# Performance work log

Measured on AMD Instinct MI355X. Metric: run time of the kernel, lower is better.

## Reference

```python
import jax, jax.numpy as jnp
import numpy as np

NA, NB, NG = 40000, 200000, 500000
D, H, IN = 64, 64, 256  # feature dim, gMLP hidden, concat input dim (64+2*64+64)


def silu(x):
    return x * jax.nn.sigmoid(x)


def setup_inputs() -> dict:
    key = jax.random.key(0)
    ks = jax.random.split(key, 16)
    n = lambda k, sh, s=0.05: jax.random.normal(k, sh, jnp.float32) * s
    return {
        "atom_feas": n(ks[0], (NA, D), 1.0),
        "bond_feas": n(ks[1], (NB, D), 1.0),
        "bond_weights": jax.random.uniform(ks[2], (NB, D), jnp.float32),
        "angle_feas": n(ks[3], (NG, D), 1.0),
        "bond_graph": jax.random.randint(ks[4], (NG, 3), 0, NA, jnp.int64
                                          if jax.config.jax_enable_x64 else jnp.int32),
        "Wc1": n(ks[5], (IN, H)), "bc1": jnp.zeros((H,), jnp.float32),
        "Wc2": n(ks[6], (H, D)), "bc2": jnp.zeros((D,), jnp.float32),
        "Wg1": n(ks[7], (IN, H)), "bg1": jnp.zeros((H,), jnp.float32),
        "Wg2": n(ks[8], (H, D)), "bg2": jnp.zeros((D,), jnp.float32),
        "Wo": n(ks[9], (D, D)), "bo": jnp.zeros((D,), jnp.float32),
    }


def reference(atom_feas, bond_feas, bond_weights, angle_feas, bond_graph,
              Wc1, bc1, Wc2, bc2, Wg1, bg1, Wg2, bg2, Wo, bo):
    ci = bond_graph[:, 0]  # center atom index
    bi = bond_graph[:, 1]  # bond i index (also scatter target)
    bj = bond_graph[:, 2]  # bond j index
    # gather -> concat: [NG, 2*D + D + D] = [NG, 256]
    total = jnp.concatenate(
        [bond_feas[bi], bond_feas[bj], angle_feas, atom_feas[ci]], axis=1)
    # gated MLP (norm=None path): core = act(mlp_core(x)), gate = sigmoid(mlp_gate(x))
    core = silu(silu(total @ Wc1 + bc1) @ Wc2 + bc2)
    gate = jax.nn.sigmoid(silu(total @ Wg1 + bg1) @ Wg2 + bg2)
    upd = core * gate * bond_weights[bi] * bond_weights[bj]
    # scatter-sum back onto bonds (aggregate with average=False)
    agg = jax.ops.segment_sum(upd, bi, num_segments=bond_feas.shape[0])
    # mlp_out (single Linear) + residual; bond_norm is None
    return agg @ Wo + bo + bond_feas
```

## Files before the change

### kernel.cpp

```cpp
#include <hip/hip_runtime.h>
#include <hip/hip_bf16.h>

static constexpr int KD  = 64;
static constexpr int KH  = 64;

typedef __attribute__((ext_vector_type(8))) short bf16x8;
typedef __attribute__((ext_vector_type(4))) float f32x4;
typedef __attribute__((ext_vector_type(2))) float f32x2;

__device__ inline unsigned short f2bf(float f) {
  union { float f; unsigned u; } uf; uf.f = f;
  unsigned u = uf.u;
  return (unsigned short)((u + 0x7FFFu + ((u >> 16) & 1u)) >> 16);
}
__device__ inline float bf2f(unsigned short h) {
  union { unsigned u; float f; } x; x.u = ((unsigned)h) << 16; return x.f;
}
__device__ inline unsigned cvtpk_bf16(float lo, float hi) {
  unsigned r;
  asm("v_cvt_pk_bf16_f32 %0, %1, %2" : "=v"(r) : "v"(lo), "v"(hi));
  return r;
}
__device__ inline bf16x8 pack8(const float* p) {
  float4 lo = *(const float4*)p;
  float4 hi = *(const float4*)(p + 4);
  union { unsigned u[4]; bf16x8 v; } t;
  t.u[0] = cvtpk_bf16(lo.x, lo.y);
  t.u[1] = cvtpk_bf16(lo.z, lo.w);
  t.u[2] = cvtpk_bf16(hi.x, hi.y);
  t.u[3] = cvtpk_bf16(hi.z, hi.w);
  return t.v;
}
__device__ inline float sigm(float x) {
  return __builtin_amdgcn_rcpf(1.0f + __expf(-x));
}
__device__ inline float silu_(float x) { return x * sigm(x); }
__device__ inline unsigned pk_fp8x4(float a0, float a1, float a2, float a3) {
  int v = __builtin_amdgcn_cvt_pk_fp8_f32(a0, a1, 0, false);
  v = __builtin_amdgcn_cvt_pk_fp8_f32(a2, a3, v, true);
  return (unsigned)v;
}
template<bool HI>
__device__ inline f32x2 sum3_fp8(unsigned a, unsigned b, unsigned c) {
  f32x2 A = __builtin_amdgcn_cvt_pk_f32_fp8((int)a, HI);
  f32x2 B = __builtin_amdgcn_cvt_pk_f32_fp8((int)b, HI);
  f32x2 C = __builtin_amdgcn_cvt_pk_f32_fp8((int)c, HI);
  return (A + B) + C;
}
__device__ inline int quad_off(int n, int p) {
  return ((n >> 1) << 5) + (p << 3) + ((n & 1) << 2);
}

__global__ void k_prep(const float* __restrict__ wc1, const float* __restrict__ wg1,
                       const float* __restrict__ wc2, const float* __restrict__ wg2,
                       const float* __restrict__ wo,
                       const float* __restrict__ bc1, const float* __restrict__ bg1,
                       unsigned short* __restrict__ wpb, unsigned short* __restrict__ wpa,
                       unsigned short* __restrict__ wpg,
                       unsigned short* __restrict__ wc2t, unsigned short* __restrict__ wg2t,
                       unsigned short* __restrict__ wot, float* __restrict__ biaspg,
                       const int* __restrict__ bgr, int* __restrict__ cnt, int ng) {
  int t = blockIdx.x * 256 + threadIdx.x;
  if (t < 16384) {
    int blk = t >> 9, n = blk >> 1, s = blk & 1;
    int lane = (t >> 3) & 63, e = t & 7;
    int p = lane >> 4, q = lane & 15;
    int k = 32 * s + 8 * p + e;
    int o = 16 * n + q;
    float v;
    if (o < 64)       v = wc1[k * KH + o];
    else if (o < 128) v = wg1[k * KH + (o - 64)];
    else if (o < 192) v = wc1[(64 + k) * KH + (o - 128)];
    else              v = wg1[(64 + k) * KH + (o - 192)];
    wpb[t] = f2bf(v);
  }
  if (t < 8192) {
    int blk = t >> 9, n = blk >> 1, s = blk & 1;
    int lane = (t >> 3) & 63, e = t & 7;
    int p = lane >> 4, q = lane & 15;
    int k = 32 * s + 8 * p + e;
    int o = 16 * n + q;
    float va = (o < 64) ? wc1[(192 + k) * KH + o] : wg1[(192 + k) * KH + (o - 64)];
    wpa[t] = f2bf(va);
    float vg = (o < 64) ? wc1[(128 + k) * KH + o] : wg1[(128 + k) * KH + (o - 64)];
    wpg[t] = f2bf(vg);
  }
  if (t < KH * KD) {
    int d = t >> 6, kp = t & 63;
    int h = 32 * (kp >> 5) + 16 * ((kp >> 2) & 1) + 4 * ((kp >> 3) & 3) + (kp & 3);
    wc2t[t] = f2bf(wc2[h * KD + d]);
    wg2t[t] = f2bf(wg2[h * KD + d]);
    wot[t]  = f2bf(wo[kp * KD + d]);
  }
  if (t < 128) biaspg[t] = (t < 64) ? bc1[t] : bg1[t - 64];
  if (t < ng) atomicAdd(&cnt[bgr[3 * t + 1]], 1);
}

template<int NOUT>
__global__ __launch_bounds__(256) void k_partial(
    const float* __restrict__ X, const unsigned short* __restrict__ wfrag,
    unsigned char* __restrict__ P, int nrows,
    int rowstride, const float* __restrict__ bwsrc) {
  constexpr int NSH = NOUT * 64;
  __shared__ unsigned short wl[NSH];
  const int tid = threadIdx.x;
  for (int c = tid * 8; c < NSH; c += 256 * 8)
    *(bf16x8*)&wl[c] = *(const bf16x8*)&wfrag[c];
  __syncthreads();
  const int wave = tid >> 6, lane = tid & 63, p = lane >> 4, q = lane & 15;
  const int ntile = (nrows + 63) >> 6;
  for (int tile = blockIdx.x; tile < ntile; tile += gridDim.x) {
    const int r0 = tile * 64 + wave * 16 + q;
    const int r = (r0 < nrows) ? r0 : (nrows - 1);
    bf16x8 b[2];
    b[0] = pack8(X + (long)r * 64 + 8 * p);
    b[1] = pack8(X + (long)r * 64 + 32 + 8 * p);
    unsigned char* dst = P + (long)r0 * rowstride;
#pragma unroll
    for (int n = 0; n < NOUT / 16; n++) {
      f32x4 acc = (f32x4){0.f, 0.f, 0.f, 0.f};
#pragma unroll
      for (int s = 0; s < 2; s++) {
        bf16x8 a = *(const bf16x8*)&wl[((n * 2 + s) * 64 + lane) * 8];
        acc = __builtin_amdgcn_mfma_f32_16x16x32_bf16(a, b[s], acc, 0, 0, 0);
      }
      if (r0 < nrows) {
        const int po = ((n >> 2) << 6) + quad_off(n & 3, p);
        *(unsigned*)(dst + po) = pk_fp8x4(acc[0], acc[1], acc[2], acc[3]);
      }
    }
    if (bwsrc != nullptr && r0 < nrows) {
#pragma unroll
      for (int n = 0; n < 4; n++) {
        float4 w = *(const float4*)(bwsrc + (long)r0 * 64 + 16 * n + 4 * p);
        *(unsigned*)(dst + 256 + quad_off(n, p)) = pk_fp8x4(w.x, w.y, w.z, w.w);
      }
    }
  }
}

__global__ __launch_bounds__(256) void k_scan1(const int* __restrict__ cnt,
                                               int* __restrict__ part,
                                               int* __restrict__ bsum, int n) {
  __shared__ int wsum[4];
  const int tid = threadIdx.x;
  const int i = blockIdx.x * 256 + tid;
  const int lane = tid & 63, w = tid >> 6;
  int orig = (i < n) ? cnt[i] : 0;
  int v = orig;
#pragma unroll
  for (int d = 1; d < 64; d <<= 1) {
    int t = __shfl_up(v, d);
    if (lane >= d) v += t;
  }
  if (lane == 63) wsum[w] = v;
  __syncthreads();
  int add = 0;
  for (int k = 0; k < w; k++) add += wsum[k];
  v += add;
  if (i < n) part[i] = v - orig;
  if (tid == 255) bsum[blockIdx.x] = v;
}

__global__ __launch_bounds__(1024) void k_scan2(const int* __restrict__ bsum,
                                                int* __restrict__ bscan, int nblk) {
  __shared__ int wsum[16];
  const int tid = threadIdx.x;
  const int lane = tid & 63, w = tid >> 6;
  int orig = (tid < nblk) ? bsum[tid] : 0;
  int v = orig;
#pragma unroll
  for (int d = 1; d < 64; d <<= 1) {
    int t = __shfl_up(v, d);
    if (lane >= d) v += t;
  }
  if (lane == 63) wsum[w] = v;
  __syncthreads();
  int add = 0;
  for (int k = 0; k < w; k++) add += wsum[k];
  v += add;
  if (tid < nblk) bscan[tid] = v - orig;
}

__global__ void k_scan3(const int* __restrict__ part, const int* __restrict__ bscan,
                        int* __restrict__ off, int* __restrict__ cur, int n) {
  int i = blockIdx.x * blockDim.x + threadIdx.x;
  if (i < n) {
    off[i] = part[i] + bscan[i >> 8];
    cur[i] = 0;
  }
}

__global__ __launch_bounds__(256) void k_fused(
    const float* __restrict__ ang, const unsigned short* __restrict__ wfrag,
    const float* __restrict__ biaspg, const int* __restrict__ bgr,
    const int* __restrict__ off, int* __restrict__ cur,
    const unsigned char* __restrict__ PBX, const unsigned char* __restrict__ PA,
    const unsigned short* __restrict__ wc2t, const unsigned short* __restrict__ wg2t,
    const float* __restrict__ bc2, const float* __restrict__ bg2,
    unsigned short* __restrict__ upd2, int ng) {
  __shared__ unsigned short wl[128 * 64];
  const int tid = threadIdx.x;
  for (int c = tid * 8; c < 128 * 64; c += 256 * 8)
    *(bf16x8*)&wl[c] = *(const bf16x8*)&wfrag[c];
  __syncthreads();
  const int wave = tid >> 6, lane = tid & 63, p = lane >> 4, q = lane & 15;
  const int ntile = (ng + 63) >> 6;
  const int p8 = p << 3;

  int tile = blockIdx.x;
  int ci, bi, bj;
  {
    const int g0 = tile * 64 + wave * 16 + q;
    const int g = (g0 < ng) ? g0 : (ng - 1);
    ci = bgr[3 * g]; bi = bgr[3 * g + 1]; bj = bgr[3 * g + 2];
  }
  for (; tile < ntile; tile += gridDim.x) {
    const int g0 = tile * 64 + wave * 16 + q;
    const bool ok = g0 < ng;
    const int g = ok ? g0 : (ng - 1);

    int nci = ci, nbi = bi, nbj = bj;
    const int tnext = tile + gridDim.x;
    if (tnext < ntile) {
      const int g0n = tnext * 64 + wave * 16 + q;
      const int gn = (g0n < ng) ? g0n : (ng - 1);
      nci = bgr[3 * gn]; nbi = bgr[3 * gn + 1]; nbj = bgr[3 * gn + 2];
    }

    int rr = 0;
    if (p == 0 && ok) {
      int slot = atomicAdd(&cur[bi], 1);
      rr = off[bi] + slot;
    }
    rr = __shfl(rr, q);

    const unsigned char* rb1 = PBX + (long)bi * 384;
    const unsigned char* rb2 = PBX + (long)bj * 384 + 128;
    const unsigned char* ra  = PA + (long)ci * 128;

    uint2 c1[2], c2[2], c3[2];
#pragma unroll
    for (int np = 0; np < 2; np++) {
      const int o = (np << 5) + p8;
      c1[np] = *(const uint2*)(rb1 + o);
      c2[np] = *(const uint2*)(rb2 + o);
      c3[np] = *(const uint2*)(ra + o);
    }
    bf16x8 b0 = pack8(ang + (long)g * 64 + p8);
    bf16x8 b1 = pack8(ang + (long)g * 64 + 32 + p8);

    f32x4 h[4];
#pragma unroll
    for (int n = 0; n < 4; n++)
      h[n] = (f32x4&)*(const float4*)(biaspg + 16 * n + 4 * p);
#pragma unroll
    for (int n = 0; n < 4; n++) {
      bf16x8 a0 = *(const bf16x8*)&wl[((n * 2 + 0) * 64 + lane) * 8];
      h[n] = __builtin_amdgcn_mfma_f32_16x16x32_bf16(a0, b0, h[n], 0, 0, 0);
      bf16x8 a1 = *(const bf16x8*)&wl[((n * 2 + 1) * 64 + lane) * 8];
      h[n] = __builtin_amdgcn_mfma_f32_16x16x32_bf16(a1, b1, h[n], 0, 0, 0);
    }
#pragma unroll
    for (int np = 0; np < 2; np++) {
      f32x2 lo = sum3_fp8<false>(c1[np].x, c2[np].x, c3[np].x);
      f32x2 hi = sum3_fp8<true >(c1[np].x, c2[np].x, c3[np].x);
      h[2*np][0] += lo[0]; h[2*np][1] += lo[1]; h[2*np][2] += hi[0]; h[2*np][3] += hi[1];
      lo = sum3_fp8<false>(c1[np].y, c2[np].y, c3[np].y);
      hi = sum3_fp8<true >(c1[np].y, c2[np].y, c3[np].y);
      h[2*np+1][0] += lo[0]; h[2*np+1][1] += lo[1]; h[2*np+1][2] += hi[0]; h[2*np+1][3] += hi[1];
    }
    bf16x8 b2f[2];
#pragma unroll
    for (int s2 = 0; s2 < 2; s2++) {
      union { unsigned u[4]; bf16x8 v; } t;
#pragma unroll
      for (int eh = 0; eh < 4; eh++) {
        const int e0 = 2 * eh;
        const int n = 2 * s2 + (e0 >> 2), j = e0 & 3;
        t.u[eh] = cvtpk_bf16(silu_(h[n][j]), silu_(h[n][j + 1]));
      }
      b2f[s2] = t.v;
    }

    uint2 g1[2], g2[2], g3[2], bwp[2];
#pragma unroll
    for (int np = 0; np < 2; np++) {
      const int o = 64 + (np << 5) + p8;
      g1[np] = *(const uint2*)(rb1 + o);
      g2[np] = *(const uint2*)(rb2 + o);
      g3[np] = *(const uint2*)(ra + o);
      bwp[np] = *(const uint2*)(rb2 + 128 + (np << 5) + p8);
    }

    f32x4 o4[4];
#pragma unroll
    for (int n2 = 0; n2 < 4; n2++)
      o4[n2] = (f32x4&)*(const float4*)(bc2 + 16 * n2 + 4 * p);
#pragma unroll
    for (int s2 = 0; s2 < 2; s2++) {
      const int ko = 32 * s2 + p8;
#pragma unroll
      for (int n2 = 0; n2 < 4; n2++) {
        bf16x8 a1 = *(const bf16x8*)(wc2t + (q + 16 * n2) * KH + ko);
        o4[n2] = __builtin_amdgcn_mfma_f32_16x16x32_bf16(a1, b2f[s2], o4[n2], 0, 0, 0);
      }
    }
    float sc[16];
#pragma unroll
    for (int n2 = 0; n2 < 4; n2++)
#pragma unroll
      for (int j = 0; j < 4; j++)
        sc[4 * n2 + j] = silu_(o4[n2][j]);

#pragma unroll
    for (int n = 0; n < 4; n++)
      h[n] = (f32x4&)*(const float4*)(biaspg + 64 + 16 * n + 4 * p);
#pragma unroll
    for (int n = 0; n < 4; n++) {
      bf16x8 a0 = *(const bf16x8*)&wl[(((4 + n) * 2 + 0) * 64 + lane) * 8];
      h[n] = __builtin_amdgcn_mfma_f32_16x16x32_bf16(a0, b0, h[n], 0, 0, 0);
      bf16x8 a1 = *(const bf16x8*)&wl[(((4 + n) * 2 + 1) * 64 + lane) * 8];
      h[n] = __builtin_amdgcn_mfma_f32_16x16x32_bf16(a1, b1, h[n], 0, 0, 0);
    }
#pragma unroll
    for (int np = 0; np < 2; np++) {
      f32x2 lo = sum3_fp8<false>(g1[np].x, g2[np].x, g3[np].x);
      f32x2 hi = sum3_fp8<true >(g1[np].x, g2[np].x, g3[np].x);
      h[2*np][0] += lo[0]; h[2*np][1] += lo[1]; h[2*np][2] += hi[0]; h[2*np][3] += hi[1];
      lo = sum3_fp8<false>(g1[np].y, g2[np].y, g3[np].y);
      hi = sum3_fp8<true >(g1[np].y, g2[np].y, g3[np].y);
      h[2*np+1][0] += lo[0]; h[2*np+1][1] += lo[1]; h[2*np+1][2] += hi[0]; h[2*np+1][3] += hi[1];
    }
#pragma unroll
    for (int s2 = 0; s2 < 2; s2++) {
      union { unsigned u[4]; bf16x8 v; } t;
#pragma unroll
      for (int eh = 0; eh < 4; eh++) {
        const int e0 = 2 * eh;
        const int n = 2 * s2 + (e0 >> 2), j = e0 & 3;
        t.u[eh] = cvtpk_bf16(silu_(h[n][j]), silu_(h[n][j + 1]));
      }
      b2f[s2] = t.v;
    }
    f32x4 og[4];
#pragma unroll
    for (int n2 = 0; n2 < 4; n2++)
      og[n2] = (f32x4&)*(const float4*)(bg2 + 16 * n2 + 4 * p);
#pragma unroll
    for (int s2 = 0; s2 < 2; s2++) {
      const int ko = 32 * s2 + p8;
#pragma unroll
      for (int n2 = 0; n2 < 4; n2++) {
        bf16x8 a2 = *(const bf16x8*)(wg2t + (q + 16 * n2) * KH + ko);
        og[n2] = __builtin_amdgcn_mfma_f32_16x16x32_bf16(a2, b2f[s2], og[n2], 0, 0, 0);
      }
    }

    if (ok) {
      unsigned short* dst = upd2 + (long)rr * KD;
#pragma unroll
      for (int n2 = 0; n2 < 4; n2++) {
        const unsigned w = (n2 & 1) ? bwp[n2 >> 1].y : bwp[n2 >> 1].x;
        f32x2 blo = __builtin_amdgcn_cvt_pk_f32_fp8((int)w, false);
        f32x2 bhi = __builtin_amdgcn_cvt_pk_f32_fp8((int)w, true);
        float f0 = sc[4 * n2 + 0] * sigm(og[n2][0]) * blo[0];
        float f1 = sc[4 * n2 + 1] * sigm(og[n2][1]) * blo[1];
        float f2 = sc[4 * n2 + 2] * sigm(og[n2][2]) * bhi[0];
        float f3 = sc[4 * n2 + 3] * sigm(og[n2][3]) * bhi[1];
        uint2 st;
        st.x = cvtpk_bf16(f0, f1);
        st.y = cvtpk_bf16(f2, f3);
        *(uint2*)(dst + 16 * n2 + 4 * p) = st;
      }
    }
    ci = nci; bi = nbi; bj = nbj;
  }
}

__global__ __launch_bounds__(256) void k_aggout(
    const float* __restrict__ bond, const float* __restrict__ bwt,
    const unsigned short* __restrict__ upd2,
    const int* __restrict__ off, const int* __restrict__ cnt,
    const unsigned short* __restrict__ wot, const float* __restrict__ bo,
    float* __restrict__ out, int na, int nb) {
  const int wave = threadIdx.x >> 6;
  const int lane = threadIdx.x & 63;
  const int r15 = lane & 15;
  const int ck = lane >> 4;
  const int base = blockIdx.x * 64 + wave * 16;
  const int b = base + r15;
  const bool hasseg = (b < na);
  const int bc = hasseg ? b : 0;
  const int o = off[bc];
  const int c = hasseg ? cnt[bc] : 0;
  const int d0 = ck * 8;

  float acc[16];
#pragma unroll
  for (int e = 0; e < 16; e++) acc[e] = 0.0f;

  int it = 0;
  for (; it + 2 <= c; it += 2) {
    const unsigned short* r0 = upd2 + (long)(o + it) * KD;
    const unsigned short* r1 = r0 + KD;
    bf16x8 l0 = *(const bf16x8*)(r0 + d0);
    bf16x8 h0 = *(const bf16x8*)(r0 + 32 + d0);
    bf16x8 l1 = *(const bf16x8*)(r1 + d0);
    bf16x8 h1 = *(const bf16x8*)(r1 + 32 + d0);
#pragma unroll
    for (int e = 0; e < 8; e++) {
      acc[e]     += bf2f((unsigned short)l0[e]) + bf2f((unsigned short)l1[e]);
      acc[8 + e] += bf2f((unsigned short)h0[e]) + bf2f((unsigned short)h1[e]);
    }
  }
  if (it < c) {
    const unsigned short* r0 = upd2 + (long)(o + it) * KD;
    bf16x8 l0 = *(const bf16x8*)(r0 + d0);
    bf16x8 h0 = *(const bf16x8*)(r0 + 32 + d0);
#pragma unroll
    for (int e = 0; e < 8; e++) {
      acc[e]     += bf2f((unsigned short)l0[e]);
      acc[8 + e] += bf2f((unsigned short)h0[e]);
    }
  }

  if (hasseg) {
    const float* w = bwt + (long)b * KD;
    float4 w0 = *(const float4*)(w + d0);
    float4 w1 = *(const float4*)(w + d0 + 4);
    float4 w2 = *(const float4*)(w + 32 + d0);
    float4 w3 = *(const float4*)(w + 32 + d0 + 4);
    acc[0] *= w0.x;  acc[1] *= w0.y;  acc[2] *= w0.z;  acc[3] *= w0.w;
    acc[4] *= w1.x;  acc[5] *= w1.y;  acc[6] *= w1.z;  acc[7] *= w1.w;
    acc[8] *= w2.x;  acc[9] *= w2.y;  acc[10] *= w2.z; acc[11] *= w2.w;
    acc[12] *= w3.x; acc[13] *= w3.y; acc[14] *= w3.z; acc[15] *= w3.w;
  }

  bf16x8 a[2];
  {
    union { unsigned u[4]; bf16x8 v; } t0, t1;
    t0.u[0] = cvtpk_bf16(acc[0], acc[1]);
    t0.u[1] = cvtpk_bf16(acc[2], acc[3]);
    t0.u[2] = cvtpk_bf16(acc[4], acc[5]);
    t0.u[3] = cvtpk_bf16(acc[6], acc[7]);
    t1.u[0] = cvtpk_bf16(acc[8], acc[9]);
    t1.u[1] = cvtpk_bf16(acc[10], acc[11]);
    t1.u[2] = cvtpk_bf16(acc[12], acc[13]);
    t1.u[3] = cvtpk_bf16(acc[14], acc[15]);
    a[0] = t0.v;
    a[1] = t1.v;
  }

  f32x4 acc2[4];
#pragma unroll
  for (int n = 0; n < 4; n++) {
    float bv = bo[n * 16 + r15];
    acc2[n] = (f32x4){bv, bv, bv, bv};
  }
#pragma unroll
  for (int s = 0; s < 2; s++) {
    const int koff = s * 32 + ck * 8;
#pragma unroll
    for (int n = 0; n < 4; n++) {
      bf16x8 bf = *(const bf16x8*)(wot + (n * 16 + r15) * KH + koff);
      acc2[n] = __builtin_amdgcn_mfma_f32_16x16x32_bf16(a[s], bf, acc2[n], 0, 0, 0);
    }
  }
#pragma unroll
  for (int n = 0; n < 4; n++) {
#pragma unroll
    for (int j = 0; j < 4; j++) {
      const int orow = base + ck * 4 + j;
      if (orow < nb) {
        const int d = n * 16 + r15;
        out[(long)orow * KD + d] = acc2[n][j] + bond[(long)orow * KD + d];
      }
    }
  }
}

extern "C" void kernel_launch(void* const* d_in, const int* in_sizes, int n_in,
                              void* d_out, int out_size, void* d_ws, size_t ws_size,
                              hipStream_t stream) {
  const float* atom = (const float*)d_in[0];
  const float* bond = (const float*)d_in[1];
  const float* bwt  = (const float*)d_in[2];
  const float* ang  = (const float*)d_in[3];
  const int*   bgr  = (const int*)d_in[4];
  const float* wc1 = (const float*)d_in[5];
  const float* bc1 = (const float*)d_in[6];
  const float* wc2 = (const float*)d_in[7];
  const float* bc2 = (const float*)d_in[8];
  const float* wg1 = (const float*)d_in[9];
  const float* bg1 = (const float*)d_in[10];
  const float* wg2 = (const float*)d_in[11];
  const float* bg2 = (const float*)d_in[12];
  const float* wo  = (const float*)d_in[13];
  const float* bo  = (const float*)d_in[14];

  const int na = in_sizes[0] / KD;
  const int nb = in_sizes[1] / KD;
  const int ng = in_sizes[4] / 3;
  float* out = (float*)d_out;

  char* pp = (char*)d_ws;
  auto alloc = [&](size_t bytes) { char* r = pp; pp += (bytes + 255) & ~(size_t)255; return r; };
  unsigned short* wpb  = (unsigned short*)alloc(16384 * 2);
  unsigned short* wpa  = (unsigned short*)alloc(8192 * 2);
  unsigned short* wpg  = (unsigned short*)alloc(8192 * 2);
  unsigned short* wc2t = (unsigned short*)alloc((size_t)KH * KD * 2);
  unsigned short* wg2t = (unsigned short*)alloc((size_t)KH * KD * 2);
  unsigned short* wot  = (unsigned short*)alloc((size_t)KH * KD * 2);
  float* biaspg        = (float*)alloc(128 * 4);
  unsigned char* PBX   = (unsigned char*)alloc((size_t)na * 384);
  unsigned char* PA    = (unsigned char*)alloc((size_t)na * 128);
  unsigned short* upd2 = (unsigned short*)alloc((size_t)ng * KD * 2);
  int* cnt  = (int*)alloc((size_t)na * 4);
  int* cur  = (int*)alloc((size_t)na * 4);
  int* offb = (int*)alloc((size_t)na * 4);
  int* part = (int*)alloc((size_t)na * 4);
  int* bsum  = (int*)alloc(4096);
  int* bscan = (int*)alloc(4096);

  const int nblk = (na + 255) / 256;

  hipMemsetAsync(cnt, 0, (size_t)na * 4, stream);

  k_prep<<<(ng + 255) / 256, 256, 0, stream>>>(wc1, wg1, wc2, wg2, wo, bc1, bg1,
                                               wpb, wpa, wpg, wc2t, wg2t, wot, biaspg,
                                               bgr, cnt, ng);
  k_scan1<<<nblk, 256, 0, stream>>>(cnt, part, bsum, na);
  k_scan2<<<1, 1024, 0, stream>>>(bsum, bscan, nblk);
  k_scan3<<<nblk, 256, 0, stream>>>(part, bscan, offb, cur, na);

  const int tb = (na + 63) / 64;
  k_partial<256><<<tb, 256, 0, stream>>>(bond, wpb, PBX, na, 384, bwt);
  k_partial<128><<<tb, 256, 0, stream>>>(atom, wpa, PA, na, 128, (const float*)nullptr);

  k_fused<<<2048, 256, 0, stream>>>(ang, wpg, biaspg, bgr, offb, cur,
                                    PBX, PA, wc2t, wg2t, bc2, bg2, upd2, ng);

  k_aggout<<<(nb + 63) / 64, 256, 0, stream>>>(bond, bwt, upd2, offb, cnt,
                                               wot, bo, out, na, nb);
}
```

Measured before the change: 270.0 us.

## Widen fp8 partial-row gathers to 16-byte loads and issue them early

Changes the byte layout of the precomputed fp8 partial rows (quad_off) so each lane's four n-values sit contiguously, letting the fused kernel fetch core, gate and bond-weight partials with single 16-byte loads instead of several 8-byte loads. All gathers, including the angle rows, are moved to the top of the loop so their latency overlaps the atomic slot reservation and the first MFMAs. The grid of the fused kernel is also doubled. This raises register pressure from holding the loaded data longer, and it depends on k_prep/k_partial writing the new layout consistently.

```diff
diff --git a/kernel.cpp b/kernel.cpp
--- a/kernel.cpp
+++ b/kernel.cpp
@@ -7,6 +7,7 @@
 typedef __attribute__((ext_vector_type(8))) short bf16x8;
 typedef __attribute__((ext_vector_type(4))) float f32x4;
 typedef __attribute__((ext_vector_type(2))) float f32x2;
+typedef __attribute__((ext_vector_type(4))) unsigned u32x4;
 
 __device__ inline unsigned short f2bf(float f) {
   union { float f; unsigned u; } uf; uf.f = f;
@@ -48,7 +49,7 @@
   return (A + B) + C;
 }
 __device__ inline int quad_off(int n, int p) {
-  return ((n >> 1) << 5) + (p << 3) + ((n & 1) << 2);
+  return (p << 4) + (n << 2);
 }
 
 __global__ void k_prep(const float* __restrict__ wc1, const float* __restrict__ wg1,
@@ -207,6 +208,7 @@
   const int wave = tid >> 6, lane = tid & 63, p = lane >> 4, q = lane & 15;
   const int ntile = (ng + 63) >> 6;
   const int p8 = p << 3;
+  const int p16 = p << 4;
 
   int tile = blockIdx.x;
   int ci, bi, bj;
@@ -220,6 +222,21 @@
     const bool ok = g0 < ng;
     const int g = ok ? g0 : (ng - 1);
 
+    const unsigned char* rb1 = PBX + (long)bi * 384;
+    const unsigned char* rb2 = PBX + (long)bj * 384 + 128;
+    const unsigned char* ra  = PA + (long)ci * 128;
+
+    u32x4 c1 = *(const u32x4*)(rb1 + p16);
+    u32x4 g1 = *(const u32x4*)(rb1 + 64 + p16);
+    u32x4 c2 = *(const u32x4*)(rb2 + p16);
+    u32x4 g2 = *(const u32x4*)(rb2 + 64 + p16);
+    u32x4 ca = *(const u32x4*)(ra + p16);
+    u32x4 ga = *(const u32x4*)(ra + 64 + p16);
+    u32x4 bw = *(const u32x4*)(rb2 + 128 + p16);
+
+    bf16x8 b0 = pack8(ang + (long)g * 64 + p8);
+    bf16x8 b1 = pack8(ang + (long)g * 64 + 32 + p8);
+
     int nci = ci, nbi = bi, nbj = bj;
     const int tnext = tile + gridDim.x;
     if (tnext < ntile) {
@@ -235,21 +252,6 @@
     }
     rr = __shfl(rr, q);
 
-    const unsigned char* rb1 = PBX + (long)bi * 384;
-    const unsigned char* rb2 = PBX + (long)bj * 384 + 128;
-    const unsigned char* ra  = PA + (long)ci * 128;
-
-    uint2 c1[2], c2[2], c3[2];
-#pragma unroll
-    for (int np = 0; np < 2; np++) {
-      const int o = (np << 5) + p8;
-      c1[np] = *(const uint2*)(rb1 + o);
-      c2[np] = *(const uint2*)(rb2 + o);
-      c3[np] = *(const uint2*)(ra + o);
-    }
-    bf16x8 b0 = pack8(ang + (long)g * 64 + p8);
-    bf16x8 b1 = pack8(ang + (long)g * 64 + 32 + p8);
-
     f32x4 h[4];
 #pragma unroll
     for (int n = 0; n < 4; n++)
@@ -262,13 +264,10 @@
       h[n] = __builtin_amdgcn_mfma_f32_16x16x32_bf16(a1, b1, h[n], 0, 0, 0);
     }
 #pragma unroll
-    for (int np = 0; np < 2; np++) {
-      f32x2 lo = sum3_fp8<false>(c1[np].x, c2[np].x, c3[np].x);
-      f32x2 hi = sum3_fp8<true >(c1[np].x, c2[np].x, c3[np].x);
-      h[2*np][0] += lo[0]; h[2*np][1] += lo[1]; h[2*np][2] += hi[0]; h[2*np][3] += hi[1];
-      lo = sum3_fp8<false>(c1[np].y, c2[np].y, c3[np].y);
-      hi = sum3_fp8<true >(c1[np].y, c2[np].y, c3[np].y);
-      h[2*np+1][0] += lo[0]; h[2*np+1][1] += lo[1]; h[2*np+1][2] += hi[0]; h[2*np+1][3] += hi[1];
+    for (int n = 0; n < 4; n++) {
+      f32x2 lo = sum3_fp8<false>(c1[n], c2[n], ca[n]);
+      f32x2 hi = sum3_fp8<true >(c1[n], c2[n], ca[n]);
+      h[n][0] += lo[0]; h[n][1] += lo[1]; h[n][2] += hi[0]; h[n][3] += hi[1];
     }
     bf16x8 b2f[2];
 #pragma unroll
@@ -281,16 +280,6 @@
         t.u[eh] = cvtpk_bf16(silu_(h[n][j]), silu_(h[n][j + 1]));
       }
       b2f[s2] = t.v;
-    }
-
-    uint2 g1[2], g2[2], g3[2], bwp[2];
-#pragma unroll
-    for (int np = 0; np < 2; np++) {
-      const int o = 64 + (np << 5) + p8;
-      g1[np] = *(const uint2*)(rb1 + o);
-      g2[np] = *(const uint2*)(rb2 + o);
-      g3[np] = *(const uint2*)(ra + o);
-      bwp[np] = *(const uint2*)(rb2 + 128 + (np << 5) + p8);
     }
 
     f32x4 o4[4];
@@ -324,13 +313,10 @@
       h[n] = __builtin_amdgcn_mfma_f32_16x16x32_bf16(a1, b1, h[n], 0, 0, 0);
     }
 #pragma unroll
-    for (int np = 0; np < 2; np++) {
-      f32x2 lo = sum3_fp8<false>(g1[np].x, g2[np].x, g3[np].x);
-      f32x2 hi = sum3_fp8<true >(g1[np].x, g2[np].x, g3[np].x);
-      h[2*np][0] += lo[0]; h[2*np][1] += lo[1]; h[2*np][2] += hi[0]; h[2*np][3] += hi[1];
-      lo = sum3_fp8<false>(g1[np].y, g2[np].y, g3[np].y);
-      hi = sum3_fp8<true >(g1[np].y, g2[np].y, g3[np].y);
-      h[2*np+1][0] += lo[0]; h[2*np+1][1] += lo[1]; h[2*np+1][2] += hi[0]; h[2*np+1][3] += hi[1];
+    for (int n = 0; n < 4; n++) {
+      f32x2 lo = sum3_fp8<false>(g1[n], g2[n], ga[n]);
+      f32x2 hi = sum3_fp8<true >(g1[n], g2[n], ga[n]);
+      h[n][0] += lo[0]; h[n][1] += lo[1]; h[n][2] += hi[0]; h[n][3] += hi[1];
     }
 #pragma unroll
     for (int s2 = 0; s2 < 2; s2++) {
@@ -361,9 +347,8 @@
       unsigned short* dst = upd2 + (long)rr * KD;
 #pragma unroll
       for (int n2 = 0; n2 < 4; n2++) {
-        const unsigned w = (n2 & 1) ? bwp[n2 >> 1].y : bwp[n2 >> 1].x;
-        f32x2 blo = __builtin_amdgcn_cvt_pk_f32_fp8((int)w, false);
-        f32x2 bhi = __builtin_amdgcn_cvt_pk_f32_fp8((int)w, true);
+        f32x2 blo = __builtin_amdgcn_cvt_pk_f32_fp8((int)bw[n2], false);
+        f32x2 bhi = __builtin_amdgcn_cvt_pk_f32_fp8((int)bw[n2], true);
         float f0 = sc[4 * n2 + 0] * sigm(og[n2][0]) * blo[0];
         float f1 = sc[4 * n2 + 1] * sigm(og[n2][1]) * blo[1];
         float f2 = sc[4 * n2 + 2] * sigm(og[n2][2]) * bhi[0];
@@ -538,7 +523,7 @@
   k_partial<256><<<tb, 256, 0, stream>>>(bond, wpb, PBX, na, 384, bwt);
   k_partial<128><<<tb, 256, 0, stream>>>(atom, wpa, PA, na, 128, (const float*)nullptr);
 
-  k_fused<<<2048, 256, 0, stream>>>(ang, wpg, biaspg, bgr, offb, cur,
+  k_fused<<<4096, 256, 0, stream>>>(ang, wpg, biaspg, bgr, offb, cur,
                                     PBX, PA, wc2t, wg2t, bc2, bg2, upd2, ng);
 
   k_aggout<<<(nb + 63) / 64, 256, 0, stream>>>(bond, bwt, upd2, offb, cnt,
```

New measurement: 248.9 us. -7.8%, faster.
